# Performance work log

Hardware: AMD Instinct MI355X
Metric: run time of the kernel (lower is better)

The kernel has to match this reference:

```python
import jax, jax.numpy as jnp
import numpy as np

EMBED_DIM = 256
NUM_HEADS = 8
HEAD_DIM = EMBED_DIM // NUM_HEADS
ADJ_CHANNELS = 4
B, N = 8, 1024


def setup_inputs() -> dict:
    key = jax.random.key(0)
    ks = jax.random.split(key, 12)
    s = 1.0 / np.sqrt(EMBED_DIM)
    sa = 1.0 / np.sqrt(ADJ_CHANNELS)
    return {
        "x": jax.random.normal(ks[0], (B, N, EMBED_DIM), dtype=jnp.float32),
        "adj": jax.random.uniform(ks[1], (B, N, N, ADJ_CHANNELS), dtype=jnp.float32),
        "Wq": jax.random.uniform(ks[2], (EMBED_DIM, EMBED_DIM), jnp.float32, -s, s),
        "bq": jnp.zeros((EMBED_DIM,), jnp.float32),
        "Wk": jax.random.uniform(ks[3], (EMBED_DIM, EMBED_DIM), jnp.float32, -s, s),
        "bk": jnp.zeros((EMBED_DIM,), jnp.float32),
        "Wv": jax.random.uniform(ks[4], (EMBED_DIM, EMBED_DIM), jnp.float32, -s, s),
        "bv": jnp.zeros((EMBED_DIM,), jnp.float32),
        "Wo": jax.random.uniform(ks[5], (EMBED_DIM, EMBED_DIM), jnp.float32, -s, s),
        "bo": jnp.zeros((EMBED_DIM,), jnp.float32),
        "Wa": jax.random.uniform(ks[6], (ADJ_CHANNELS, NUM_HEADS), jnp.float32, -sa, sa),
        "ba": jnp.zeros((NUM_HEADS,), jnp.float32),
    }


def reference(x, adj, Wq, bq, Wk, bk, Wv, bv, Wo, bo, Wa, ba):
    Bs, Ns, E = x.shape
    H, D = NUM_HEADS, HEAD_DIM
    def heads(W, b):
        return (x @ W + b).reshape(Bs, Ns, H, D).transpose(0, 2, 1, 3)  # [B,H,N,D]
    Q, K, V = heads(Wq, bq), heads(Wk, bk), heads(Wv, bv)
    # adjacency-derived additive bias: [B,N,N,C] -> [B,N,N,H] -> [B,H,N,N]
    bias = jnp.moveaxis(adj @ Wa + ba, -1, 1)
    scores = jnp.einsum("bhnd,bhmd->bhnm", Q, K) / np.sqrt(D) + bias
    attn = jax.nn.softmax(scores, axis=-1)
    ctx = jnp.einsum("bhnm,bhmd->bhnd", attn, V)  # [B,H,N,D]
    ctx = ctx.transpose(0, 2, 1, 3).reshape(Bs, Ns, E)
    return ctx @ Wo + bo + x
```

## Files before the change

### kernel.cpp

```cpp
#include <hip/hip_runtime.h>
#include <hip/hip_bf16.h>

#define BATCH 8
#define SEQ   1024
#define EMB   256
#define NH    8
#define HD    32
#define QSCALE 0.2550030053f

typedef __attribute__((ext_vector_type(8))) short short8;
typedef __attribute__((ext_vector_type(4))) float floatx4;

__device__ __forceinline__ ushort f2bf(float f) {
    __hip_bfloat16 h = __float2bfloat16(f);
    return *reinterpret_cast<ushort*>(&h);
}

__device__ __forceinline__ float bf2f(ushort u) {
    unsigned v = ((unsigned)u) << 16;
    return __builtin_bit_cast(float, v);
}

__device__ __forceinline__ void gload_lds16(const float4* g, float4* l) {
    __builtin_amdgcn_global_load_lds(
        (const __attribute__((address_space(1))) unsigned int*)g,
        (__attribute__((address_space(3))) unsigned int*)l, 16, 0, 0);
}


__global__ __launch_bounds__(256) void prep_kernel(
    const float* __restrict__ Wq, const float* __restrict__ Wk,
    const float* __restrict__ Wv, const float* __restrict__ Wo,
    const float* __restrict__ x,
    ushort* __restrict__ Wqt, ushort* __restrict__ Wkt,
    ushort* __restrict__ Wvt, ushort* __restrict__ Wot,
    ushort* __restrict__ xb)
{
    const int blk = blockIdx.x;
    if (blk < 256) {
        __shared__ float tilebuf[32][33];
        const int mat = blk >> 6, tile = blk & 63;
        const int ti = tile >> 3, tj = tile & 7;
        const float* W = (mat == 0) ? Wq : (mat == 1) ? Wk : (mat == 2) ? Wv : Wo;
        ushort* Wt = (mat == 0) ? Wqt : (mat == 1) ? Wkt : (mat == 2) ? Wvt : Wot;
        const float scale = (mat == 0) ? QSCALE : 1.0f;

        const int tx = threadIdx.x & 31, ty = threadIdx.x >> 5;
        #pragma unroll
        for (int p = 0; p < 4; ++p)
            tilebuf[ty + p * 8][tx] = W[(size_t)(ti * 32 + ty + p * 8) * EMB + tj * 32 + tx];
        __syncthreads();
        #pragma unroll
        for (int p = 0; p < 4; ++p) {
            const int n = tj * 32 + ty + p * 8;
            const int k = ti * 32 + tx;
            Wt[(size_t)(n >> 4) * 4096 + (k >> 5) * 512 + ((k >> 3) & 3) * 128
               + (n & 15) * 8 + (k & 7)] = f2bf(tilebuf[tx][ty + p * 8] * scale);
        }
    } else {
        const int tile = blk - 256;
        const float* __restrict__ xs = x + (size_t)tile * 16 * EMB;
        ushort* __restrict__ xd = xb + (size_t)tile * 4096;
        #pragma unroll
        for (int j = 0; j < 16; ++j) {
            const int o = j * 256 + threadIdx.x;
            const int ks = o >> 9, quad = (o >> 7) & 3, l16 = (o >> 3) & 15, e = o & 7;
            xd[o] = f2bf(xs[(size_t)l16 * EMB + ks * 32 + quad * 8 + e]);
        }
    }
}

__global__ __launch_bounds__(256) void qkv_gemm(
    const ushort* __restrict__ xb,
    const ushort* __restrict__ Wqt, const ushort* __restrict__ Wkt,
    const ushort* __restrict__ Wvt,
    const float* __restrict__ bq, const float* __restrict__ bk,
    const float* __restrict__ bv,
    ushort* __restrict__ Qb, ushort* __restrict__ Kb, ushort* __restrict__ Vt)
{
    const int mat = blockIdx.y;
    const ushort* __restrict__ Wt = (mat == 0) ? Wqt : (mat == 1) ? Wkt : Wvt;
    const float* __restrict__ bias = (mat == 0) ? bq : (mat == 1) ? bk : bv;
    const float bscale = (mat == 0) ? QSCALE : 1.0f;

    const int w = threadIdx.x >> 6, lane = threadIdx.x & 63;
    const int quad = lane >> 4, l16 = lane & 15;
    const int row0 = blockIdx.x * 64 + w * 16;

    floatx4 acc[16];
    #pragma unroll
    for (int i = 0; i < 16; ++i) acc[i] = (floatx4){0.f, 0.f, 0.f, 0.f};

    const ushort* __restrict__ xrow = xb + (size_t)(blockIdx.x * 4 + w) * 4096 + lane * 8;
    const ushort* __restrict__ wrow = Wt + lane * 8;

    #pragma unroll
    for (int ks = 0; ks < 8; ++ks) {
        const short8 a = *(const short8*)(xrow + ks * 512);
        #pragma unroll
        for (int i = 0; i < 16; ++i) {
            const short8 bf = *(const short8*)(wrow + (size_t)i * 4096 + ks * 512);
            acc[i] = __builtin_amdgcn_mfma_f32_16x16x32_bf16(a, bf, acc[i], 0, 0, 0);
        }
    }

    const int gr0 = row0 + quad * 4;
    if (mat < 2) {
        ushort* __restrict__ dst = (mat == 0) ? Qb : Kb;
        #pragma unroll
        for (int i = 0; i < 16; ++i) {
            const int c = i * 16 + l16, h = c >> 5, d = c & (HD - 1);
            const float bb = bias[c] * bscale;
            #pragma unroll
            for (int r = 0; r < 4; ++r) {
                const int gr = gr0 + r, b = gr >> 10, n = gr & (SEQ - 1);
                dst[(size_t)(b * NH + h) * SEQ * HD + (size_t)(n >> 4) * 512
                    + (d >> 3) * 128 + (n & 15) * 8 + (d & 7)] = f2bf(acc[i][r] + bb);
            }
        }
    } else {
        const int b = gr0 >> 10, n0 = gr0 & (SEQ - 1);
        const int keyblk = n0 >> 5, j0 = n0 & 31;
        const int sg = (j0 & 15) >> 2, si0 = (j0 & 16) ? 4 : 0;
        #pragma unroll
        for (int i = 0; i < 16; ++i) {
            const int c = i * 16 + l16, h = c >> 5, d = c & (HD - 1);
            const float bb = bias[c];
            ushort4 t4;
            t4.x = f2bf(acc[i][0] + bb); t4.y = f2bf(acc[i][1] + bb);
            t4.z = f2bf(acc[i][2] + bb); t4.w = f2bf(acc[i][3] + bb);
            *(ushort4*)(Vt + (size_t)(b * NH + h) * SEQ * HD + (size_t)keyblk * 1024
                        + (d >> 4) * 512 + sg * 128 + (d & 15) * 8 + si0) = t4;
        }
    }
}

__global__ __launch_bounds__(512) void attn_kernel(
    const ushort* __restrict__ Qb, const ushort* __restrict__ Kb,
    const ushort* __restrict__ Vt, const float* __restrict__ adj,
    const float* __restrict__ Wa, const float* __restrict__ ba,
    ushort* __restrict__ cp, float* __restrict__ lsum)
{
    __shared__ float4 Atile[2][16][65];
    const int tid = threadIdx.x, h = tid >> 6, lane = tid & 63;
    const int quad = lane >> 4, l16 = lane & 15;
    const int q0 = blockIdx.x * 16, b = blockIdx.y, z = blockIdx.z;
    const int bh = b * NH + h;
    const int kz = z * 512;

    const float LOG2E = 1.4426950408889634f;
    const float wa0 = Wa[0 * NH + h] * LOG2E, wa1 = Wa[1 * NH + h] * LOG2E;
    const float wa2 = Wa[2 * NH + h] * LOG2E, wa3 = Wa[3 * NH + h] * LOG2E;
    const float bah = ba[h] * LOG2E;

    const short8 aq = *(const short8*)(Qb + (size_t)bh * SEQ * HD
                                      + (size_t)blockIdx.x * 512 + lane * 8);

    floatx4 o0 = {0.f, 0.f, 0.f, 0.f}, o1 = {0.f, 0.f, 0.f, 0.f};
    float lacc = 0.f;

    const float4* __restrict__ adjb = (const float4*)adj + (size_t)b * SEQ * SEQ;
    const float4* __restrict__ asrc0 = adjb + (size_t)(q0 + 2 * h)     * SEQ + kz + lane;
    const float4* __restrict__ asrc1 = adjb + (size_t)(q0 + 2 * h + 1) * SEQ + kz + lane;

    const ushort* __restrict__ Kbase = Kb + (size_t)bh * SEQ * HD + lane * 8;
    const ushort* __restrict__ Vbase = Vt + (size_t)bh * SEQ * HD + lane * 8;

    gload_lds16(asrc0, &Atile[0][2 * h][0]);
    gload_lds16(asrc1, &Atile[0][2 * h + 1][0]);
    __syncthreads();

    for (int it = 0; it < 8; ++it) {
        const int cur = it & 1;
        const int key0 = kz + it * 64;

        if (it < 7) {
            gload_lds16(asrc0 + (it + 1) * 64, &Atile[cur ^ 1][2 * h][0]);
            gload_lds16(asrc1 + (it + 1) * 64, &Atile[cur ^ 1][2 * h + 1][0]);
        }

        const ushort* kp = Kbase + (size_t)(key0 >> 4) * 512;
        const short8 k0 = *(const short8*)(kp);
        const short8 k1 = *(const short8*)(kp + 512);
        const short8 k2 = *(const short8*)(kp + 1024);
        const short8 k3 = *(const short8*)(kp + 1536);
        const floatx4 zz = {0.f, 0.f, 0.f, 0.f};
        floatx4 s0 = __builtin_amdgcn_mfma_f32_16x16x32_bf16(k0, aq, zz, 0, 0, 0);
        floatx4 s1 = __builtin_amdgcn_mfma_f32_16x16x32_bf16(k1, aq, zz, 0, 0, 0);
        floatx4 s2 = __builtin_amdgcn_mfma_f32_16x16x32_bf16(k2, aq, zz, 0, 0, 0);
        floatx4 s3 = __builtin_amdgcn_mfma_f32_16x16x32_bf16(k3, aq, zz, 0, 0, 0);

        ushort pu0[8], pu1[8];
        #pragma unroll
        for (int r = 0; r < 4; ++r) {
            const int col = 4 * quad + r;
            const float4 a0 = Atile[cur][l16][col];
            const float4 a1 = Atile[cur][l16][16 + col];
            const float4 a2 = Atile[cur][l16][32 + col];
            const float4 a3 = Atile[cur][l16][48 + col];
            const float b0 = fmaf(a0.x, wa0, fmaf(a0.y, wa1, fmaf(a0.z, wa2, fmaf(a0.w, wa3, bah))));
            const float b1 = fmaf(a1.x, wa0, fmaf(a1.y, wa1, fmaf(a1.z, wa2, fmaf(a1.w, wa3, bah))));
            const float b2 = fmaf(a2.x, wa0, fmaf(a2.y, wa1, fmaf(a2.z, wa2, fmaf(a2.w, wa3, bah))));
            const float b3 = fmaf(a3.x, wa0, fmaf(a3.y, wa1, fmaf(a3.z, wa2, fmaf(a3.w, wa3, bah))));
            const float p0 = __builtin_amdgcn_exp2f(s0[r] + b0);
            const float p1 = __builtin_amdgcn_exp2f(s1[r] + b1);
            const float p2 = __builtin_amdgcn_exp2f(s2[r] + b2);
            const float p3 = __builtin_amdgcn_exp2f(s3[r] + b3);
            lacc += (p0 + p1) + (p2 + p3);
            pu0[r]     = f2bf(p0);
            pu0[4 + r] = f2bf(p1);
            pu1[r]     = f2bf(p2);
            pu1[4 + r] = f2bf(p3);
        }
        const short8 pf0 = *(const short8*)pu0;
        const short8 pf1 = *(const short8*)pu1;

        const ushort* vp = Vbase + (size_t)(key0 >> 5) * 1024;
        const short8 v00 = *(const short8*)(vp);
        const short8 v10 = *(const short8*)(vp + 512);
        const short8 v01 = *(const short8*)(vp + 1024);
        const short8 v11 = *(const short8*)(vp + 1536);
        o0 = __builtin_amdgcn_mfma_f32_16x16x32_bf16(v00, pf0, o0, 0, 0, 0);
        o1 = __builtin_amdgcn_mfma_f32_16x16x32_bf16(v10, pf0, o1, 0, 0, 0);
        o0 = __builtin_amdgcn_mfma_f32_16x16x32_bf16(v01, pf1, o0, 0, 0, 0);
        o1 = __builtin_amdgcn_mfma_f32_16x16x32_bf16(v11, pf1, o1, 0, 0, 0);

        __syncthreads();
    }

    lacc += __shfl_xor(lacc, 16, 64);
    lacc += __shfl_xor(lacc, 32, 64);

    ushort* __restrict__ cpz = cp + (size_t)z * BATCH * SEQ * EMB;
    float* __restrict__ lsz = lsum + (size_t)z * BATCH * SEQ * NH;
    const size_t tbase = ((size_t)b * 64 + blockIdx.x) * 4096 + (size_t)h * 512
                       + l16 * 32 + 4 * quad;
    ushort4 t0, t1;
    t0.x = f2bf(o0[0]); t0.y = f2bf(o0[1]); t0.z = f2bf(o0[2]); t0.w = f2bf(o0[3]);
    t1.x = f2bf(o1[0]); t1.y = f2bf(o1[1]); t1.z = f2bf(o1[2]); t1.w = f2bf(o1[3]);
    *(ushort4*)(cpz + tbase)      = t0;
    *(ushort4*)(cpz + tbase + 16) = t1;
    const size_t grow = (size_t)b * SEQ + q0 + l16;
    if (quad == 0) lsz[grow * NH + h] = lacc;
}

__global__ __launch_bounds__(256) void outproj_gemm(
    const ushort* __restrict__ cp, const float* __restrict__ lsum,
    const ushort* __restrict__ Wot, const float* __restrict__ bo,
    const float* __restrict__ x, float* __restrict__ out)
{
    const int w = threadIdx.x >> 6, lane = threadIdx.x & 63;
    const int quad = lane >> 4, l16 = lane & 15;
    const int row0 = blockIdx.x * 64 + w * 16;
    const int c0 = blockIdx.y * 128;
    const int arow = row0 + l16;
    const ushort* __restrict__ cp1 = cp + (size_t)BATCH * SEQ * EMB;
    const float* __restrict__ l1  = lsum + (size_t)BATCH * SEQ * NH;

    const size_t tb = (size_t)(blockIdx.x * 4 + w) * 4096 + l16 * 32 + quad * 8;
    const ushort* __restrict__ wrow = Wot + (size_t)(c0 >> 4) * 4096 + lane * 8;

    floatx4 acc[8];
    #pragma unroll
    for (int i = 0; i < 8; ++i) acc[i] = (floatx4){0.f, 0.f, 0.f, 0.f};

    #pragma unroll
    for (int ks = 0; ks < 8; ++ks) {
        const float invl = 1.0f / (lsum[(size_t)arow * NH + ks] + l1[(size_t)arow * NH + ks]);
        const ushort4 c00 = *(const ushort4*)(cp  + tb + ks * 512);
        const ushort4 c01 = *(const ushort4*)(cp  + tb + ks * 512 + 4);
        const ushort4 c10 = *(const ushort4*)(cp1 + tb + ks * 512);
        const ushort4 c11 = *(const ushort4*)(cp1 + tb + ks * 512 + 4);
        ushort au[8] = {
            f2bf((bf2f(c00.x) + bf2f(c10.x)) * invl),
            f2bf((bf2f(c00.y) + bf2f(c10.y)) * invl),
            f2bf((bf2f(c00.z) + bf2f(c10.z)) * invl),
            f2bf((bf2f(c00.w) + bf2f(c10.w)) * invl),
            f2bf((bf2f(c01.x) + bf2f(c11.x)) * invl),
            f2bf((bf2f(c01.y) + bf2f(c11.y)) * invl),
            f2bf((bf2f(c01.z) + bf2f(c11.z)) * invl),
            f2bf((bf2f(c01.w) + bf2f(c11.w)) * invl)};
        const short8 a = *(const short8*)au;
        #pragma unroll
        for (int i = 0; i < 8; ++i) {
            const short8 bfr = *(const short8*)(wrow + (size_t)i * 4096 + ks * 512);
            acc[i] = __builtin_amdgcn_mfma_f32_16x16x32_bf16(a, bfr, acc[i], 0, 0, 0);
        }
    }

    const int gr0 = row0 + quad * 4;
    #pragma unroll
    for (int i = 0; i < 8; ++i) {
        const int c = c0 + i * 16 + l16;
        const float bov = bo[c];
        #pragma unroll
        for (int r = 0; r < 4; ++r) {
            const size_t idx = (size_t)(gr0 + r) * EMB + c;
            out[idx] = acc[i][r] + bov + x[idx];
        }
    }
}

extern "C" void kernel_launch(void* const* d_in, const int* in_sizes, int n_in,
                              void* d_out, int out_size, void* d_ws, size_t ws_size,
                              hipStream_t stream) {
    const float* x   = (const float*)d_in[0];
    const float* adj = (const float*)d_in[1];
    const float* Wq  = (const float*)d_in[2];
    const float* bq  = (const float*)d_in[3];
    const float* Wk  = (const float*)d_in[4];
    const float* bk  = (const float*)d_in[5];
    const float* Wv  = (const float*)d_in[6];
    const float* bv  = (const float*)d_in[7];
    const float* Wo  = (const float*)d_in[8];
    const float* bo  = (const float*)d_in[9];
    const float* Wa  = (const float*)d_in[10];
    const float* ba  = (const float*)d_in[11];

    const size_t per = (size_t)BATCH * NH * SEQ * HD;
    ushort* Qb  = (ushort*)d_ws;
    ushort* Kb  = Qb + per;
    ushort* Vt  = Kb + per;
    ushort* Wqt = Vt + per;
    ushort* Wkt = Wqt + EMB * EMB;
    ushort* Wvt = Wkt + EMB * EMB;
    ushort* Wot = Wvt + EMB * EMB;
    ushort* cpw = Wot + EMB * EMB;
    ushort* xbp = cpw + 2 * (size_t)BATCH * SEQ * EMB;
    float*  ls  = (float*)(xbp + (size_t)BATCH * SEQ * EMB);

    prep_kernel<<<768, 256, 0, stream>>>(Wq, Wk, Wv, Wo, x,
                                         Wqt, Wkt, Wvt, Wot, xbp);
    qkv_gemm<<<dim3(BATCH * SEQ / 64, 3), 256, 0, stream>>>(
        xbp, Wqt, Wkt, Wvt, bq, bk, bv, Qb, Kb, Vt);
    attn_kernel<<<dim3(SEQ / 16, BATCH, 2), 512, 0, stream>>>(
        Qb, Kb, Vt, adj, Wa, ba, cpw, ls);
    outproj_gemm<<<dim3(BATCH * SEQ / 64, 2), 256, 0, stream>>>(
        cpw, ls, Wot, bo, x, (float*)d_out);
}
```

Before: 276.0 us.

## Process two 16-query tiles per attention block to reuse K/V loads

Each attention block now handles 32 queries instead of 16, loading K and V fragments once per iteration and feeding two sets of MFMAs with them. The adjacency tile in LDS doubles, the grid halves, and the launch bounds add a minimum-occupancy hint. This is meant to halve K/V global traffic per query and amortize per-block overhead. In exchange it raises register and LDS use and gives fewer blocks to hide latency.

```diff
diff --git a/kernel.cpp b/kernel.cpp
--- a/kernel.cpp
+++ b/kernel.cpp
@@ -135,16 +135,16 @@
     }
 }
 
-__global__ __launch_bounds__(512) void attn_kernel(
+__global__ __launch_bounds__(512, 4) void attn_kernel(
     const ushort* __restrict__ Qb, const ushort* __restrict__ Kb,
     const ushort* __restrict__ Vt, const float* __restrict__ adj,
     const float* __restrict__ Wa, const float* __restrict__ ba,
     ushort* __restrict__ cp, float* __restrict__ lsum)
 {
-    __shared__ float4 Atile[2][16][65];
+    __shared__ float4 Atile[2][32][65];
     const int tid = threadIdx.x, h = tid >> 6, lane = tid & 63;
     const int quad = lane >> 4, l16 = lane & 15;
-    const int q0 = blockIdx.x * 16, b = blockIdx.y, z = blockIdx.z;
+    const int q0 = blockIdx.x * 32, b = blockIdx.y, z = blockIdx.z;
     const int bh = b * NH + h;
     const int kz = z * 512;
 
@@ -153,21 +153,26 @@
     const float wa2 = Wa[2 * NH + h] * LOG2E, wa3 = Wa[3 * NH + h] * LOG2E;
     const float bah = ba[h] * LOG2E;
 
-    const short8 aq = *(const short8*)(Qb + (size_t)bh * SEQ * HD
-                                      + (size_t)blockIdx.x * 512 + lane * 8);
-
-    floatx4 o0 = {0.f, 0.f, 0.f, 0.f}, o1 = {0.f, 0.f, 0.f, 0.f};
-    float lacc = 0.f;
+    const ushort* __restrict__ qbase = Qb + (size_t)bh * SEQ * HD + lane * 8;
+    const short8 aqA = *(const short8*)(qbase + (size_t)(blockIdx.x * 2)     * 512);
+    const short8 aqB = *(const short8*)(qbase + (size_t)(blockIdx.x * 2 + 1) * 512);
+
+    floatx4 oA0 = {0.f, 0.f, 0.f, 0.f}, oA1 = {0.f, 0.f, 0.f, 0.f};
+    floatx4 oB0 = {0.f, 0.f, 0.f, 0.f}, oB1 = {0.f, 0.f, 0.f, 0.f};
+    float laccA = 0.f, laccB = 0.f;
 
     const float4* __restrict__ adjb = (const float4*)adj + (size_t)b * SEQ * SEQ;
-    const float4* __restrict__ asrc0 = adjb + (size_t)(q0 + 2 * h)     * SEQ + kz + lane;
-    const float4* __restrict__ asrc1 = adjb + (size_t)(q0 + 2 * h + 1) * SEQ + kz + lane;
+    const float4* asrc[4];
+    #pragma unroll
+    for (int p = 0; p < 4; ++p)
+        asrc[p] = adjb + (size_t)(q0 + 4 * h + p) * SEQ + kz + lane;
 
     const ushort* __restrict__ Kbase = Kb + (size_t)bh * SEQ * HD + lane * 8;
     const ushort* __restrict__ Vbase = Vt + (size_t)bh * SEQ * HD + lane * 8;
 
-    gload_lds16(asrc0, &Atile[0][2 * h][0]);
-    gload_lds16(asrc1, &Atile[0][2 * h + 1][0]);
+    #pragma unroll
+    for (int p = 0; p < 4; ++p)
+        gload_lds16(asrc[p], &Atile[0][4 * h + p][0]);
     __syncthreads();
 
     for (int it = 0; it < 8; ++it) {
@@ -175,8 +180,9 @@
         const int key0 = kz + it * 64;
 
         if (it < 7) {
-            gload_lds16(asrc0 + (it + 1) * 64, &Atile[cur ^ 1][2 * h][0]);
-            gload_lds16(asrc1 + (it + 1) * 64, &Atile[cur ^ 1][2 * h + 1][0]);
+            #pragma unroll
+            for (int p = 0; p < 4; ++p)
+                gload_lds16(asrc[p] + (it + 1) * 64, &Atile[cur ^ 1][4 * h + p][0]);
         }
 
         const ushort* kp = Kbase + (size_t)(key0 >> 4) * 512;
@@ -185,63 +191,101 @@
         const short8 k2 = *(const short8*)(kp + 1024);
         const short8 k3 = *(const short8*)(kp + 1536);
         const floatx4 zz = {0.f, 0.f, 0.f, 0.f};
-        floatx4 s0 = __builtin_amdgcn_mfma_f32_16x16x32_bf16(k0, aq, zz, 0, 0, 0);
-        floatx4 s1 = __builtin_amdgcn_mfma_f32_16x16x32_bf16(k1, aq, zz, 0, 0, 0);
-        floatx4 s2 = __builtin_amdgcn_mfma_f32_16x16x32_bf16(k2, aq, zz, 0, 0, 0);
-        floatx4 s3 = __builtin_amdgcn_mfma_f32_16x16x32_bf16(k3, aq, zz, 0, 0, 0);
-
-        ushort pu0[8], pu1[8];
+        floatx4 sA0 = __builtin_amdgcn_mfma_f32_16x16x32_bf16(k0, aqA, zz, 0, 0, 0);
+        floatx4 sA1 = __builtin_amdgcn_mfma_f32_16x16x32_bf16(k1, aqA, zz, 0, 0, 0);
+        floatx4 sA2 = __builtin_amdgcn_mfma_f32_16x16x32_bf16(k2, aqA, zz, 0, 0, 0);
+        floatx4 sA3 = __builtin_amdgcn_mfma_f32_16x16x32_bf16(k3, aqA, zz, 0, 0, 0);
+        floatx4 sB0 = __builtin_amdgcn_mfma_f32_16x16x32_bf16(k0, aqB, zz, 0, 0, 0);
+        floatx4 sB1 = __builtin_amdgcn_mfma_f32_16x16x32_bf16(k1, aqB, zz, 0, 0, 0);
+        floatx4 sB2 = __builtin_amdgcn_mfma_f32_16x16x32_bf16(k2, aqB, zz, 0, 0, 0);
+        floatx4 sB3 = __builtin_amdgcn_mfma_f32_16x16x32_bf16(k3, aqB, zz, 0, 0, 0);
+
+        ushort puA0[8], puA1[8], puB0[8], puB1[8];
         #pragma unroll
         for (int r = 0; r < 4; ++r) {
             const int col = 4 * quad + r;
-            const float4 a0 = Atile[cur][l16][col];
-            const float4 a1 = Atile[cur][l16][16 + col];
-            const float4 a2 = Atile[cur][l16][32 + col];
-            const float4 a3 = Atile[cur][l16][48 + col];
-            const float b0 = fmaf(a0.x, wa0, fmaf(a0.y, wa1, fmaf(a0.z, wa2, fmaf(a0.w, wa3, bah))));
-            const float b1 = fmaf(a1.x, wa0, fmaf(a1.y, wa1, fmaf(a1.z, wa2, fmaf(a1.w, wa3, bah))));
-            const float b2 = fmaf(a2.x, wa0, fmaf(a2.y, wa1, fmaf(a2.z, wa2, fmaf(a2.w, wa3, bah))));
-            const float b3 = fmaf(a3.x, wa0, fmaf(a3.y, wa1, fmaf(a3.z, wa2, fmaf(a3.w, wa3, bah))));
-            const float p0 = __builtin_amdgcn_exp2f(s0[r] + b0);
-            const float p1 = __builtin_amdgcn_exp2f(s1[r] + b1);
-            const float p2 = __builtin_amdgcn_exp2f(s2[r] + b2);
-            const float p3 = __builtin_amdgcn_exp2f(s3[r] + b3);
-            lacc += (p0 + p1) + (p2 + p3);
-            pu0[r]     = f2bf(p0);
-            pu0[4 + r] = f2bf(p1);
-            pu1[r]     = f2bf(p2);
-            pu1[4 + r] = f2bf(p3);
-        }
-        const short8 pf0 = *(const short8*)pu0;
-        const short8 pf1 = *(const short8*)pu1;
+            {
+                const float4 a0 = Atile[cur][l16][col];
+                const float4 a1 = Atile[cur][l16][16 + col];
+                const float4 a2 = Atile[cur][l16][32 + col];
+                const float4 a3 = Atile[cur][l16][48 + col];
+                const float b0 = fmaf(a0.x, wa0, fmaf(a0.y, wa1, fmaf(a0.z, wa2, fmaf(a0.w, wa3, bah))));
+                const float b1 = fmaf(a1.x, wa0, fmaf(a1.y, wa1, fmaf(a1.z, wa2, fmaf(a1.w, wa3, bah))));
+                const float b2 = fmaf(a2.x, wa0, fmaf(a2.y, wa1, fmaf(a2.z, wa2, fmaf(a2.w, wa3, bah))));
+                const float b3 = fmaf(a3.x, wa0, fmaf(a3.y, wa1, fmaf(a3.z, wa2, fmaf(a3.w, wa3, bah))));
+                const float p0 = __builtin_amdgcn_exp2f(sA0[r] + b0);
+                const float p1 = __builtin_amdgcn_exp2f(sA1[r] + b1);
+                const float p2 = __builtin_amdgcn_exp2f(sA2[r] + b2);
+                const float p3 = __builtin_amdgcn_exp2f(sA3[r] + b3);
+                laccA += (p0 + p1) + (p2 + p3);
+                puA0[r] = f2bf(p0); puA0[4 + r] = f2bf(p1);
+                puA1[r] = f2bf(p2); puA1[4 + r] = f2bf(p3);
+            }
+            {
+                const float4 a0 = Atile[cur][16 + l16][col];
+                const float4 a1 = Atile[cur][16 + l16][16 + col];
+                const float4 a2 = Atile[cur][16 + l16][32 + col];
+                const float4 a3 = Atile[cur][16 + l16][48 + col];
+                const float b0 = fmaf(a0.x, wa0, fmaf(a0.y, wa1, fmaf(a0.z, wa2, fmaf(a0.w, wa3, bah))));
+                const float b1 = fmaf(a1.x, wa0, fmaf(a1.y, wa1, fmaf(a1.z, wa2, fmaf(a1.w, wa3, bah))));
+                const float b2 = fmaf(a2.x, wa0, fmaf(a2.y, wa1, fmaf(a2.z, wa2, fmaf(a2.w, wa3, bah))));
+                const float b3 = fmaf(a3.x, wa0, fmaf(a3.y, wa1, fmaf(a3.z, wa2, fmaf(a3.w, wa3, bah))));
+                const float p0 = __builtin_amdgcn_exp2f(sB0[r] + b0);
+                const float p1 = __builtin_amdgcn_exp2f(sB1[r] + b1);
+                const float p2 = __builtin_amdgcn_exp2f(sB2[r] + b2);
+                const float p3 = __builtin_amdgcn_exp2f(sB3[r] + b3);
+                laccB += (p0 + p1) + (p2 + p3);
+                puB0[r] = f2bf(p0); puB0[4 + r] = f2bf(p1);
+                puB1[r] = f2bf(p2); puB1[4 + r] = f2bf(p3);
+            }
+        }
+        const short8 pfA0 = *(const short8*)puA0;
+        const short8 pfA1 = *(const short8*)puA1;
+        const short8 pfB0 = *(const short8*)puB0;
+        const short8 pfB1 = *(const short8*)puB1;
 
         const ushort* vp = Vbase + (size_t)(key0 >> 5) * 1024;
         const short8 v00 = *(const short8*)(vp);
         const short8 v10 = *(const short8*)(vp + 512);
         const short8 v01 = *(const short8*)(vp + 1024);
         const short8 v11 = *(const short8*)(vp + 1536);
-        o0 = __builtin_amdgcn_mfma_f32_16x16x32_bf16(v00, pf0, o0, 0, 0, 0);
-        o1 = __builtin_amdgcn_mfma_f32_16x16x32_bf16(v10, pf0, o1, 0, 0, 0);
-        o0 = __builtin_amdgcn_mfma_f32_16x16x32_bf16(v01, pf1, o0, 0, 0, 0);
-        o1 = __builtin_amdgcn_mfma_f32_16x16x32_bf16(v11, pf1, o1, 0, 0, 0);
+        oA0 = __builtin_amdgcn_mfma_f32_16x16x32_bf16(v00, pfA0, oA0, 0, 0, 0);
+        oA1 = __builtin_amdgcn_mfma_f32_16x16x32_bf16(v10, pfA0, oA1, 0, 0, 0);
+        oA0 = __builtin_amdgcn_mfma_f32_16x16x32_bf16(v01, pfA1, oA0, 0, 0, 0);
+        oA1 = __builtin_amdgcn_mfma_f32_16x16x32_bf16(v11, pfA1, oA1, 0, 0, 0);
+        oB0 = __builtin_amdgcn_mfma_f32_16x16x32_bf16(v00, pfB0, oB0, 0, 0, 0);
+        oB1 = __builtin_amdgcn_mfma_f32_16x16x32_bf16(v10, pfB0, oB1, 0, 0, 0);
+        oB0 = __builtin_amdgcn_mfma_f32_16x16x32_bf16(v01, pfB1, oB0, 0, 0, 0);
+        oB1 = __builtin_amdgcn_mfma_f32_16x16x32_bf16(v11, pfB1, oB1, 0, 0, 0);
 
         __syncthreads();
     }
 
-    lacc += __shfl_xor(lacc, 16, 64);
-    lacc += __shfl_xor(lacc, 32, 64);
+    laccA += __shfl_xor(laccA, 16, 64);
+    laccA += __shfl_xor(laccA, 32, 64);
+    laccB += __shfl_xor(laccB, 16, 64);
+    laccB += __shfl_xor(laccB, 32, 64);
 
     ushort* __restrict__ cpz = cp + (size_t)z * BATCH * SEQ * EMB;
     float* __restrict__ lsz = lsum + (size_t)z * BATCH * SEQ * NH;
-    const size_t tbase = ((size_t)b * 64 + blockIdx.x) * 4096 + (size_t)h * 512
-                       + l16 * 32 + 4 * quad;
-    ushort4 t0, t1;
-    t0.x = f2bf(o0[0]); t0.y = f2bf(o0[1]); t0.z = f2bf(o0[2]); t0.w = f2bf(o0[3]);
-    t1.x = f2bf(o1[0]); t1.y = f2bf(o1[1]); t1.z = f2bf(o1[2]); t1.w = f2bf(o1[3]);
-    *(ushort4*)(cpz + tbase)      = t0;
-    *(ushort4*)(cpz + tbase + 16) = t1;
-    const size_t grow = (size_t)b * SEQ + q0 + l16;
-    if (quad == 0) lsz[grow * NH + h] = lacc;
+    const size_t tA = ((size_t)b * 64 + blockIdx.x * 2)     * 4096 + (size_t)h * 512
+                    + l16 * 32 + 4 * quad;
+    const size_t tB = ((size_t)b * 64 + blockIdx.x * 2 + 1) * 4096 + (size_t)h * 512
+                    + l16 * 32 + 4 * quad;
+    ushort4 t;
+    t.x = f2bf(oA0[0]); t.y = f2bf(oA0[1]); t.z = f2bf(oA0[2]); t.w = f2bf(oA0[3]);
+    *(ushort4*)(cpz + tA)      = t;
+    t.x = f2bf(oA1[0]); t.y = f2bf(oA1[1]); t.z = f2bf(oA1[2]); t.w = f2bf(oA1[3]);
+    *(ushort4*)(cpz + tA + 16) = t;
+    t.x = f2bf(oB0[0]); t.y = f2bf(oB0[1]); t.z = f2bf(oB0[2]); t.w = f2bf(oB0[3]);
+    *(ushort4*)(cpz + tB)      = t;
+    t.x = f2bf(oB1[0]); t.y = f2bf(oB1[1]); t.z = f2bf(oB1[2]); t.w = f2bf(oB1[3]);
+    *(ushort4*)(cpz + tB + 16) = t;
+    if (quad == 0) {
+        const size_t growA = (size_t)b * SEQ + q0 + l16;
+        lsz[growA * NH + h]        = laccA;
+        lsz[(growA + 16) * NH + h] = laccB;
+    }
 }
 
 __global__ __launch_bounds__(256) void outproj_gemm(
@@ -333,7 +377,7 @@
                                          Wqt, Wkt, Wvt, Wot, xbp);
     qkv_gemm<<<dim3(BATCH * SEQ / 64, 3), 256, 0, stream>>>(
         xbp, Wqt, Wkt, Wvt, bq, bk, bv, Qb, Kb, Vt);
-    attn_kernel<<<dim3(SEQ / 16, BATCH, 2), 512, 0, stream>>>(
+    attn_kernel<<<dim3(SEQ / 32, BATCH, 2), 512, 0, stream>>>(
         Qb, Kb, Vt, adj, Wa, ba, cpw, ls);
     outproj_gemm<<<dim3(BATCH * SEQ / 64, 2), 256, 0, stream>>>(
         cpw, ls, Wot, bo, x, (float*)d_out);
```

New measurement: 265.6 us. -3.8%, faster.
